# Kernel tuning notes

Hardware: AMD Instinct MI355X
Metric: run time of the kernel (lower is better)

Reference implementation:

```python
import jax, jax.numpy as jnp
import numpy as np

B, N, E, K = 8, 4096, 1, 3
F = [16, 32, 16]
MLP_HID, MLP_OUT = 64, 1


def graph_filter(x, S, h, b):
    # x: [B, Fin, N], S: [E, N, N], h: [Fout, E, K, Fin], b: [Fout, 1]
    Bx, Fin, Nx = x.shape
    Ex, Kx = h.shape[1], h.shape[2]
    cur = jnp.broadcast_to(x[:, None], (Bx, Ex, Fin, Nx))  # tap 0: z = x
    zs = [cur]
    for _ in range(Kx - 1):
        cur = jnp.einsum('enm,befm->befn', S, cur)  # diffuse one hop
        zs.append(cur)
    z = jnp.stack(zs, axis=2)  # [B, E, K, Fin, N]
    return jnp.einsum('gekf,bekfn->bgn', h, z) + b[None]  # [B, Fout, N]


def gnn_layer(x, S, h, b, n_out):
    # GraphFilter -> ReLU -> NoPool (select first n_out nodes)
    return jax.nn.relu(graph_filter(x, S, h, b))[:, :, :n_out]


def setup_inputs() -> dict:
    key = jax.random.key(0)
    ks = jax.random.split(key, 16)
    sN = np.float32(1.0 / np.sqrt(N))
    x = jax.random.normal(ks[0], (B, F[0], N), dtype=jnp.float32)
    S_clique = jax.random.normal(ks[1], (E, N, N), dtype=jnp.float32) * sN
    S_line = jax.random.normal(ks[2], (E, N, N), dtype=jnp.float32) * sN

    def w(k, fo, fi):
        s = np.float32(1.0 / np.sqrt(fi * K))
        return jax.random.normal(k, (fo, E, K, fi), dtype=jnp.float32) * s

    Wc1, bc1 = w(ks[3], F[1], F[0]), jnp.zeros((F[1], 1), jnp.float32)
    Wc2, bc2 = w(ks[4], F[2], F[1]), jnp.zeros((F[2], 1), jnp.float32)
    Wl1, bl1 = w(ks[5], F[1], F[0]), jnp.zeros((F[1], 1), jnp.float32)
    Wl2, bl2 = w(ks[6], F[2], F[1]), jnp.zeros((F[2], 1), jnp.float32)
    d_in = N * F[-1]
    Wm1 = jax.random.normal(ks[7], (MLP_HID, d_in), dtype=jnp.float32) * np.float32(1.0 / np.sqrt(d_in))
    bm1 = jnp.zeros((MLP_HID,), jnp.float32)
    Wm2 = jax.random.normal(ks[8], (MLP_OUT, MLP_HID), dtype=jnp.float32) * np.float32(1.0 / np.sqrt(MLP_HID))
    bm2 = jnp.zeros((MLP_OUT,), jnp.float32)
    return {'x': x, 'S_clique': S_clique, 'S_line': S_line,
            'Wc1': Wc1, 'bc1': bc1, 'Wc2': Wc2, 'bc2': bc2,
            'Wl1': Wl1, 'bl1': bl1, 'Wl2': Wl2, 'bl2': bl2,
            'Wm1': Wm1, 'bm1': bm1, 'Wm2': Wm2, 'bm2': bm2}


def reference(x, S_clique, S_line, Wc1, bc1, Wc2, bc2, Wl1, bl1, Wl2, bl2, Wm1, bm1, Wm2, bm2):
    # clique-expansion branch (L=2 layers)
    y = gnn_layer(x, S_clique, Wc1, bc1, N)
    y = gnn_layer(y, S_clique, Wc2, bc2, N)
    # line-expansion branch (L=2 layers)
    y = gnn_layer(y, S_line, Wl1, bl1, N)
    y = gnn_layer(y, S_line, Wl2, bl2, N)
    yFlat = y.reshape(y.shape[0], -1)  # [B, F[-1]*N] (row-major matches torch)
    h = jax.nn.relu(yFlat @ Wm1.T + bm1)
    return h @ Wm2.T + bm2  # [B, 1]
```

## Files before the change

### kernel.cpp

```cpp
#include <hip/hip_runtime.h>


#define NN 4096
#define BB 8

typedef unsigned short u16;
typedef unsigned int   u32;

typedef __attribute__((ext_vector_type(8))) short bf16x8;
typedef __attribute__((ext_vector_type(4))) float f32x4;

__device__ __forceinline__ u16 f2bf(float f) {
    union { float f; u32 i; } c; c.f = f;
    u32 i = c.i;
    u32 r = (i + 0x7FFFu + ((i >> 16) & 1u)) >> 16;
    return (u16)r;
}
__device__ __forceinline__ float bf2f(u16 u) {
    union { u32 i; float f; } c; c.i = ((u32)u) << 16; return c.f;
}

__device__ __forceinline__ void gload_lds16(const u16* g, u16* l) {
    __builtin_amdgcn_global_load_lds(
        (__attribute__((address_space(1))) void*)g,
        (__attribute__((address_space(3))) void*)l, 16, 0, 0);
}

__global__ __launch_bounds__(256) void cvt_f32_bf16(const float* __restrict__ in,
                                                    u16* __restrict__ out, int n)
{
    int i = (blockIdx.x * 256 + threadIdx.x) * 4;
    const int stride = gridDim.x * 256 * 4;
    for (; i < n; i += stride) {
        float4 v = *(const float4*)(in + i);
        ushort4 o;
        o.x = f2bf(v.x); o.y = f2bf(v.y); o.z = f2bf(v.z); o.w = f2bf(v.w);
        *(ushort4*)(out + i) = o;
    }
}

__global__ __launch_bounds__(256) void diffuse(const u16* __restrict__ Z,
                                               const u16* __restrict__ S,
                                               u16* __restrict__ Part)
{
    __shared__ u16 As[128 * 64];
    __shared__ u16 Bs[64 * 64];

    const int bx    = blockIdx.x;
    const int ntile = ((bx & 7) << 3) | (bx >> 3);
    const int nBase = ntile * 64;
    const int mBase = blockIdx.y * 128;
    const int tid   = threadIdx.x;
    const int lane  = tid & 63;
    const int wv    = tid >> 6;
    const int quad  = lane >> 4;
    const int l16   = lane & 15;

    const int kSlice = NN / (int)gridDim.z;
    const int kStart = (int)blockIdx.z * kSlice;

    const int rl   = lane >> 3;
    const int gsl  = lane & 7;
    const int gsrc = gsl ^ rl;

    f32x4 acc[2][4];
#pragma unroll
    for (int i = 0; i < 2; ++i)
#pragma unroll
        for (int j = 0; j < 4; ++j) acc[i][j] = (f32x4){0.f, 0.f, 0.f, 0.f};

    for (int k0 = kStart; k0 < kStart + kSlice; k0 += 64) {
#pragma unroll
        for (int j = 0; j < 4; ++j) {
            const int rb = (wv * 4 + j) * 8;
            gload_lds16(Z + (size_t)(mBase + rb + rl) * NN + k0 + gsrc * 8,
                        &As[rb * 64]);
        }
#pragma unroll
        for (int j = 0; j < 2; ++j) {
            const int rb = (wv * 2 + j) * 8;
            gload_lds16(S + (size_t)(nBase + rb + rl) * NN + k0 + gsrc * 8,
                        &Bs[rb * 64]);
        }
        __syncthreads();

#pragma unroll
        for (int s = 0; s < 2; ++s) {
            const int g = s * 4 + quad;
            bf16x8 af[2], bf[4];
#pragma unroll
            for (int mi = 0; mi < 2; ++mi) {
                const int r = wv * 32 + mi * 16 + l16;
                af[mi] = *(const bf16x8*)&As[r * 64 + ((g ^ (r & 7)) << 3)];
            }
#pragma unroll
            for (int ni = 0; ni < 4; ++ni) {
                const int r = ni * 16 + l16;
                bf[ni] = *(const bf16x8*)&Bs[r * 64 + ((g ^ (r & 7)) << 3)];
            }
#pragma unroll
            for (int mi = 0; mi < 2; ++mi)
#pragma unroll
                for (int ni = 0; ni < 4; ++ni)
                    acc[mi][ni] = __builtin_amdgcn_mfma_f32_16x16x32_bf16(
                        af[mi], bf[ni], acc[mi][ni], 0, 0, 0);
        }
        __syncthreads();
    }

    const size_t plane = (size_t)gridDim.y * 128 * NN;
    u16* pp = Part + (size_t)blockIdx.z * plane;
#pragma unroll
    for (int mi = 0; mi < 2; ++mi)
#pragma unroll
        for (int ni = 0; ni < 4; ++ni) {
            const int row0 = mBase + wv * 32 + mi * 16 + quad * 4;
            const int col  = nBase + ni * 16 + l16;
#pragma unroll
            for (int i = 0; i < 4; ++i)
                pp[(size_t)(row0 + i) * NN + col] = f2bf(acc[mi][ni][i]);
        }
}

template <int KS>
__global__ __launch_bounds__(256) void reduce_part(const u16* __restrict__ part,
                                                   int planeElems,
                                                   u16* __restrict__ outb)
{
    const int base   = (blockIdx.x * 256 + threadIdx.x) * 8;
    const int stride = gridDim.x * 256 * 8;
    for (int i = base; i < planeElems; i += stride) {
        float s[8];
#pragma unroll
        for (int e = 0; e < 8; ++e) s[e] = 0.f;
#pragma unroll
        for (int p = 0; p < KS; ++p) {
            uint4 v = *(const uint4*)(part + (size_t)p * planeElems + i);
            const u32 w[4] = {v.x, v.y, v.z, v.w};
#pragma unroll
            for (int q = 0; q < 4; ++q) {
                union { u32 i; float f; } lo, hi;
                lo.i = w[q] << 16;
                hi.i = w[q] & 0xFFFF0000u;
                s[q * 2]     += lo.f;
                s[q * 2 + 1] += hi.f;
            }
        }
        uint4 o;
        o.x = (u32)f2bf(s[0]) | ((u32)f2bf(s[1]) << 16);
        o.y = (u32)f2bf(s[2]) | ((u32)f2bf(s[3]) << 16);
        o.z = (u32)f2bf(s[4]) | ((u32)f2bf(s[5]) << 16);
        o.w = (u32)f2bf(s[6]) | ((u32)f2bf(s[7]) << 16);
        *(uint4*)(outb + i) = o;
    }
}

template <int FIN, int FOUT>
__global__ __launch_bounds__(256) void combine_relu(
    const u16* __restrict__ z0, const u16* __restrict__ z1,
    const u16* __restrict__ z2, const float* __restrict__ W,
    const float* __restrict__ bias, u16* __restrict__ out)
{
    __shared__ float hs[FOUT * 3 * FIN];
    __shared__ float bs[FOUT];
    for (int i = threadIdx.x; i < FOUT * 3 * FIN; i += 256) hs[i] = W[i];
    if (threadIdx.x < FOUT) bs[threadIdx.x] = bias[threadIdx.x];
    __syncthreads();

    const int nb = NN / 256;
    const int b  = blockIdx.x / nb;
    const int n  = (blockIdx.x % nb) * 256 + threadIdx.x;

    float zv[3][FIN];
    const u16* zp0 = z0 + (size_t)b * FIN * NN + n;
    const u16* zp1 = z1 + (size_t)b * FIN * NN + n;
    const u16* zp2 = z2 + (size_t)b * FIN * NN + n;
#pragma unroll
    for (int f = 0; f < FIN; ++f) {
        zv[0][f] = bf2f(zp0[(size_t)f * NN]);
        zv[1][f] = bf2f(zp1[(size_t)f * NN]);
        zv[2][f] = bf2f(zp2[(size_t)f * NN]);
    }

    u16* op = out + (size_t)b * FOUT * NN + n;
    for (int g = 0; g < FOUT; ++g) {
        float acc = bs[g];
#pragma unroll
        for (int k = 0; k < 3; ++k)
#pragma unroll
            for (int f = 0; f < FIN; ++f)
                acc = fmaf(hs[(g * 3 + k) * FIN + f], zv[k][f], acc);
        op[(size_t)g * NN] = f2bf(fmaxf(acc, 0.f));
    }
}

__global__ __launch_bounds__(256) void mlp1(const u16* __restrict__ y,
                                            const float* __restrict__ Wm1,
                                            float* __restrict__ h1raw)
{
    const int j    = blockIdx.x;
    const int base = blockIdx.y * 8192;
    const int D    = 16 * NN;

    float acc[BB];
#pragma unroll
    for (int b = 0; b < BB; ++b) acc[b] = 0.f;

    const float* wrow = Wm1 + (size_t)j * D + base;
    for (int idx = threadIdx.x * 8; idx < 8192; idx += 256 * 8) {
        float4 w0 = *(const float4*)(wrow + idx);
        float4 w1 = *(const float4*)(wrow + idx + 4);
#pragma unroll
        for (int b = 0; b < BB; ++b) {
            uint4 yv = *(const uint4*)(y + (size_t)b * D + base + idx);
            union { u32 i; float f; } c[8];
            c[0].i = yv.x << 16; c[1].i = yv.x & 0xFFFF0000u;
            c[2].i = yv.y << 16; c[3].i = yv.y & 0xFFFF0000u;
            c[4].i = yv.z << 16; c[5].i = yv.z & 0xFFFF0000u;
            c[6].i = yv.w << 16; c[7].i = yv.w & 0xFFFF0000u;
            acc[b] = fmaf(w0.x, c[0].f, acc[b]);
            acc[b] = fmaf(w0.y, c[1].f, acc[b]);
            acc[b] = fmaf(w0.z, c[2].f, acc[b]);
            acc[b] = fmaf(w0.w, c[3].f, acc[b]);
            acc[b] = fmaf(w1.x, c[4].f, acc[b]);
            acc[b] = fmaf(w1.y, c[5].f, acc[b]);
            acc[b] = fmaf(w1.z, c[6].f, acc[b]);
            acc[b] = fmaf(w1.w, c[7].f, acc[b]);
        }
    }

    __shared__ float red[BB][4];
    const int lane = threadIdx.x & 63;
    const int w    = threadIdx.x >> 6;
#pragma unroll
    for (int b = 0; b < BB; ++b) {
        float v = acc[b];
        for (int off = 32; off > 0; off >>= 1) v += __shfl_down(v, off, 64);
        if (lane == 0) red[b][w] = v;
    }
    __syncthreads();
    if (threadIdx.x < BB) {
        const int b = threadIdx.x;
        atomicAdd(&h1raw[b * 64 + j],
                  red[b][0] + red[b][1] + red[b][2] + red[b][3]);
    }
}

__global__ void mlp2(const float* __restrict__ h1raw,
                     const float* __restrict__ bm1,
                     const float* __restrict__ Wm2,
                     const float* __restrict__ bm2, float* __restrict__ out)
{
    const int lane = threadIdx.x;
    const float w    = Wm2[lane];
    const float b1   = bm1[lane];
    const float bias = bm2[0];
    for (int b = 0; b < BB; ++b) {
        float v = fmaxf(h1raw[b * 64 + lane] + b1, 0.f) * w;
        for (int off = 32; off > 0; off >>= 1) v += __shfl_down(v, off, 64);
        if (lane == 0) out[b] = v + bias;
    }
}

extern "C" void kernel_launch(void* const* d_in, const int* in_sizes, int n_in,
                              void* d_out, int out_size, void* d_ws, size_t ws_size,
                              hipStream_t stream)
{
    const float* x   = (const float*)d_in[0];
    const float* Sc  = (const float*)d_in[1];
    const float* Sl  = (const float*)d_in[2];
    const float* Wc1 = (const float*)d_in[3];
    const float* bc1 = (const float*)d_in[4];
    const float* Wc2 = (const float*)d_in[5];
    const float* bc2 = (const float*)d_in[6];
    const float* Wl1 = (const float*)d_in[7];
    const float* bl1 = (const float*)d_in[8];
    const float* Wl2 = (const float*)d_in[9];
    const float* bl2 = (const float*)d_in[10];
    const float* Wm1 = (const float*)d_in[11];
    const float* bm1 = (const float*)d_in[12];
    const float* Wm2 = (const float*)d_in[13];
    const float* bm2 = (const float*)d_in[14];
    float* out = (float*)d_out;

    char* ws = (char*)d_ws;
    u16*   part = (u16*)(ws);
    u16*   zb1  = (u16*)(ws + (8u  << 20));
    u16*   zb2  = (u16*)(ws + (10u << 20));
    u16*   yPa  = (u16*)(ws + (12u << 20));
    u16*   yPb  = (u16*)(ws + (14u << 20));
    float* h1   = (float*)(ws + (16u << 20));
    u16*   Scb  = (u16*)(ws + (17u << 20));
    u16*   Slb  = Scb + (size_t)NN * NN;

    const dim3 blk(256);
    const dim3 gridCmb(BB * NN / 256);
    const dim3 g2(64, 1, 8);
    const dim3 g4(64, 2, 4);
    const int  pl128 = 128 * NN;
    const int  pl256 = 256 * NN;

    cvt_f32_bf16<<<1024, blk, 0, stream>>>(Sc, Scb, NN * NN);
    cvt_f32_bf16<<<1024, blk, 0, stream>>>(Sl, Slb, NN * NN);
    cvt_f32_bf16<<<512, blk, 0, stream>>>(x, yPa, 128 * NN);

    diffuse<<<g2, blk, 0, stream>>>(yPa, Scb, part);
    reduce_part<8><<<256, blk, 0, stream>>>(part, pl128, zb1);
    diffuse<<<g2, blk, 0, stream>>>(zb1, Scb, part);
    reduce_part<8><<<256, blk, 0, stream>>>(part, pl128, zb2);
    combine_relu<16, 32><<<gridCmb, blk, 0, stream>>>(yPa, zb1, zb2, Wc1, bc1, yPb);
    diffuse<<<g4, blk, 0, stream>>>(yPb, Scb, part);
    reduce_part<4><<<512, blk, 0, stream>>>(part, pl256, zb1);
    diffuse<<<g4, blk, 0, stream>>>(zb1, Scb, part);
    reduce_part<4><<<512, blk, 0, stream>>>(part, pl256, zb2);
    combine_relu<32, 16><<<gridCmb, blk, 0, stream>>>(yPb, zb1, zb2, Wc2, bc2, yPa);
    diffuse<<<g2, blk, 0, stream>>>(yPa, Slb, part);
    reduce_part<8><<<256, blk, 0, stream>>>(part, pl128, zb1);
    diffuse<<<g2, blk, 0, stream>>>(zb1, Slb, part);
    reduce_part<8><<<256, blk, 0, stream>>>(part, pl128, zb2);
    combine_relu<16, 32><<<gridCmb, blk, 0, stream>>>(yPa, zb1, zb2, Wl1, bl1, yPb);
    diffuse<<<g4, blk, 0, stream>>>(yPb, Slb, part);
    reduce_part<4><<<512, blk, 0, stream>>>(part, pl256, zb1);
    diffuse<<<g4, blk, 0, stream>>>(zb1, Slb, part);
    reduce_part<4><<<512, blk, 0, stream>>>(part, pl256, zb2);
    combine_relu<32, 16><<<gridCmb, blk, 0, stream>>>(yPb, zb1, zb2, Wl2, bl2, yPa);
    hipMemsetAsync(h1, 0, 64 * BB * sizeof(float), stream);
    mlp1<<<dim3(64, 8), blk, 0, stream>>>(yPa, Wm1, h1);
    mlp2<<<1, 64, 0, stream>>>(h1, bm1, Wm2, bm2, out);
}
```

Measured before the change: 399.3 us.

## Widen diffuse tile to 128x128, double split-K, fuse second reduction into combine

The diffuse GEMM tile grows from 128x64 to 128x128 with a 2x2 wave layout, so each wave computes 64x64 and the S tile is reused across more rows. Split-K depth is doubled (16 and 8 slices) to keep the grid size the same. The second-hop partial-sum reduction kernel is removed, and combine_relu now sums the split-K partials itself, which saves one launch and a round trip to memory per layer. The costs are a larger partial buffer, more accumulator registers (possibly lower occupancy), and more partial reads inside combine_relu.

```diff
diff --git a/kernel.cpp b/kernel.cpp
--- a/kernel.cpp
+++ b/kernel.cpp
@@ -44,15 +44,17 @@
                                                u16* __restrict__ Part)
 {
     __shared__ u16 As[128 * 64];
-    __shared__ u16 Bs[64 * 64];
+    __shared__ u16 Bs[128 * 64];
 
     const int bx    = blockIdx.x;
-    const int ntile = ((bx & 7) << 3) | (bx >> 3);
-    const int nBase = ntile * 64;
+    const int ntile = ((bx & 7) << 2) | (bx >> 3);
+    const int nBase = ntile * 128;
     const int mBase = blockIdx.y * 128;
     const int tid   = threadIdx.x;
     const int lane  = tid & 63;
     const int wv    = tid >> 6;
+    const int wm    = wv >> 1;
+    const int wn    = wv & 1;
     const int quad  = lane >> 4;
     const int l16   = lane & 15;
 
@@ -63,9 +65,9 @@
     const int gsl  = lane & 7;
     const int gsrc = gsl ^ rl;
 
-    f32x4 acc[2][4];
-#pragma unroll
-    for (int i = 0; i < 2; ++i)
+    f32x4 acc[4][4];
+#pragma unroll
+    for (int i = 0; i < 4; ++i)
 #pragma unroll
         for (int j = 0; j < 4; ++j) acc[i][j] = (f32x4){0.f, 0.f, 0.f, 0.f};
 
@@ -77,8 +79,8 @@
                         &As[rb * 64]);
         }
 #pragma unroll
-        for (int j = 0; j < 2; ++j) {
-            const int rb = (wv * 2 + j) * 8;
+        for (int j = 0; j < 4; ++j) {
+            const int rb = (wv * 4 + j) * 8;
             gload_lds16(S + (size_t)(nBase + rb + rl) * NN + k0 + gsrc * 8,
                         &Bs[rb * 64]);
         }
@@ -87,19 +89,19 @@
 #pragma unroll
         for (int s = 0; s < 2; ++s) {
             const int g = s * 4 + quad;
-            bf16x8 af[2], bf[4];
-#pragma unroll
-            for (int mi = 0; mi < 2; ++mi) {
-                const int r = wv * 32 + mi * 16 + l16;
+            bf16x8 af[4], bf[4];
+#pragma unroll
+            for (int mi = 0; mi < 4; ++mi) {
+                const int r = wm * 64 + mi * 16 + l16;
                 af[mi] = *(const bf16x8*)&As[r * 64 + ((g ^ (r & 7)) << 3)];
             }
 #pragma unroll
             for (int ni = 0; ni < 4; ++ni) {
-                const int r = ni * 16 + l16;
+                const int r = wn * 64 + ni * 16 + l16;
                 bf[ni] = *(const bf16x8*)&Bs[r * 64 + ((g ^ (r & 7)) << 3)];
             }
 #pragma unroll
-            for (int mi = 0; mi < 2; ++mi)
+            for (int mi = 0; mi < 4; ++mi)
 #pragma unroll
                 for (int ni = 0; ni < 4; ++ni)
                     acc[mi][ni] = __builtin_amdgcn_mfma_f32_16x16x32_bf16(
@@ -111,11 +113,11 @@
     const size_t plane = (size_t)gridDim.y * 128 * NN;
     u16* pp = Part + (size_t)blockIdx.z * plane;
 #pragma unroll
-    for (int mi = 0; mi < 2; ++mi)
+    for (int mi = 0; mi < 4; ++mi)
 #pragma unroll
         for (int ni = 0; ni < 4; ++ni) {
-            const int row0 = mBase + wv * 32 + mi * 16 + quad * 4;
-            const int col  = nBase + ni * 16 + l16;
+            const int row0 = mBase + wm * 64 + mi * 16 + quad * 4;
+            const int col  = nBase + wn * 64 + ni * 16 + l16;
 #pragma unroll
             for (int i = 0; i < 4; ++i)
                 pp[(size_t)(row0 + i) * NN + col] = f2bf(acc[mi][ni][i]);
@@ -155,10 +157,10 @@
     }
 }
 
-template <int FIN, int FOUT>
+template <int FIN, int FOUT, int KS>
 __global__ __launch_bounds__(256) void combine_relu(
     const u16* __restrict__ z0, const u16* __restrict__ z1,
-    const u16* __restrict__ z2, const float* __restrict__ W,
+    const u16* __restrict__ partz2, const float* __restrict__ W,
     const float* __restrict__ bias, u16* __restrict__ out)
 {
     __shared__ float hs[FOUT * 3 * FIN];
@@ -170,16 +172,21 @@
     const int nb = NN / 256;
     const int b  = blockIdx.x / nb;
     const int n  = (blockIdx.x % nb) * 256 + threadIdx.x;
+    const size_t plane = (size_t)BB * FIN * NN;
 
     float zv[3][FIN];
     const u16* zp0 = z0 + (size_t)b * FIN * NN + n;
     const u16* zp1 = z1 + (size_t)b * FIN * NN + n;
-    const u16* zp2 = z2 + (size_t)b * FIN * NN + n;
+    const u16* zp2 = partz2 + (size_t)b * FIN * NN + n;
 #pragma unroll
     for (int f = 0; f < FIN; ++f) {
         zv[0][f] = bf2f(zp0[(size_t)f * NN]);
         zv[1][f] = bf2f(zp1[(size_t)f * NN]);
-        zv[2][f] = bf2f(zp2[(size_t)f * NN]);
+        float s = 0.f;
+#pragma unroll
+        for (int p = 0; p < KS; ++p)
+            s += bf2f(zp2[(size_t)p * plane + (size_t)f * NN]);
+        zv[2][f] = s;
     }
 
     u16* op = out + (size_t)b * FOUT * NN + n;
@@ -285,18 +292,17 @@
 
     char* ws = (char*)d_ws;
     u16*   part = (u16*)(ws);
-    u16*   zb1  = (u16*)(ws + (8u  << 20));
-    u16*   zb2  = (u16*)(ws + (10u << 20));
-    u16*   yPa  = (u16*)(ws + (12u << 20));
-    u16*   yPb  = (u16*)(ws + (14u << 20));
-    float* h1   = (float*)(ws + (16u << 20));
-    u16*   Scb  = (u16*)(ws + (17u << 20));
+    u16*   zb1  = (u16*)(ws + (16u << 20));
+    u16*   yPa  = (u16*)(ws + (18u << 20));
+    u16*   yPb  = (u16*)(ws + (20u << 20));
+    float* h1   = (float*)(ws + (22u << 20));
+    u16*   Scb  = (u16*)(ws + (23u << 20));
     u16*   Slb  = Scb + (size_t)NN * NN;
 
     const dim3 blk(256);
     const dim3 gridCmb(BB * NN / 256);
-    const dim3 g2(64, 1, 8);
-    const dim3 g4(64, 2, 4);
+    const dim3 g2(32, 1, 16);
+    const dim3 g4(32, 2, 8);
     const int  pl128 = 128 * NN;
     const int  pl256 = 256 * NN;
 
@@ -305,25 +311,21 @@
     cvt_f32_bf16<<<512, blk, 0, stream>>>(x, yPa, 128 * NN);
 
     diffuse<<<g2, blk, 0, stream>>>(yPa, Scb, part);
-    reduce_part<8><<<256, blk, 0, stream>>>(part, pl128, zb1);
+    reduce_part<16><<<256, blk, 0, stream>>>(part, pl128, zb1);
     diffuse<<<g2, blk, 0, stream>>>(zb1, Scb, part);
-    reduce_part<8><<<256, blk, 0, stream>>>(part, pl128, zb2);
-    combine_relu<16, 32><<<gridCmb, blk, 0, stream>>>(yPa, zb1, zb2, Wc1, bc1, yPb);
+    combine_relu<16, 32, 16><<<gridCmb, blk, 0, stream>>>(yPa, zb1, part, Wc1, bc1, yPb);
     diffuse<<<g4, blk, 0, stream>>>(yPb, Scb, part);
-    reduce_part<4><<<512, blk, 0, stream>>>(part, pl256, zb1);
+    reduce_part<8><<<512, blk, 0, stream>>>(part, pl256, zb1);
     diffuse<<<g4, blk, 0, stream>>>(zb1, Scb, part);
-    reduce_part<4><<<512, blk, 0, stream>>>(part, pl256, zb2);
-    combine_relu<32, 16><<<gridCmb, blk, 0, stream>>>(yPb, zb1, zb2, Wc2, bc2, yPa);
+    combine_relu<32, 16, 8><<<gridCmb, blk, 0, stream>>>(yPb, zb1, part, Wc2, bc2, yPa);
     diffuse<<<g2, blk, 0, stream>>>(yPa, Slb, part);
-    reduce_part<8><<<256, blk, 0, stream>>>(part, pl128, zb1);
+    reduce_part<16><<<256, blk, 0, stream>>>(part, pl128, zb1);
     diffuse<<<g2, blk, 0, stream>>>(zb1, Slb, part);
-    reduce_part<8><<<256, blk, 0, stream>>>(part, pl128, zb2);
-    combine_relu<16, 32><<<gridCmb, blk, 0, stream>>>(yPa, zb1, zb2, Wl1, bl1, yPb);
+    combine_relu<16, 32, 16><<<gridCmb, blk, 0, stream>>>(yPa, zb1, part, Wl1, bl1, yPb);
     diffuse<<<g4, blk, 0, stream>>>(yPb, Slb, part);
-    reduce_part<4><<<512, blk, 0, stream>>>(part, pl256, zb1);
+    reduce_part<8><<<512, blk, 0, stream>>>(part, pl256, zb1);
     diffuse<<<g4, blk, 0, stream>>>(zb1, Slb, part);
-    reduce_part<4><<<512, blk, 0, stream>>>(part, pl256, zb2);
-    combine_relu<32, 16><<<gridCmb, blk, 0, stream>>>(yPb, zb1, zb2, Wl2, bl2, yPa);
+    combine_relu<32, 16, 8><<<gridCmb, blk, 0, stream>>>(yPb, zb1, part, Wl2, bl2, yPa);
     hipMemsetAsync(h1, 0, 64 * BB * sizeof(float), stream);
     mlp1<<<dim3(64, 8), blk, 0, stream>>>(yPa, Wm1, h1);
     mlp2<<<1, 64, 0, stream>>>(h1, bm1, Wm2, bm2, out);
```

New measurement: 410.5 us. 1.03x slower.
